# Optimization experiments

Hardware: AMD Instinct MI355X
Metric: run time of the kernel (lower is better)

The kernel has to match this reference:

```python
import jax, jax.numpy as jnp
import numpy as np

B, NPTS, NBASIS, DIM, H, CH = 8, 1024, 8, 8, 512, 16
EPSILON = 1000.0
P = 2
VOLUME = 2.0 ** DIM  # MC domain [-1,1]^dim


def setup_inputs() -> dict:
    key = jax.random.key(0)
    ks = jax.random.split(key, 10)
    s = jax.random.uniform(ks[0], (NPTS, DIM), dtype=jnp.float32) * 2.0 - 1.0  # MC samples in [-1,1]^dim
    x = jax.random.uniform(ks[1], (1, DIM), dtype=jnp.float32) * 2.0 - 1.0     # eval point
    Wfirst = jax.random.normal(ks[2], (DIM, H), dtype=jnp.float32) / np.sqrt(DIM)
    bfirst = jax.random.normal(ks[3], (H,), dtype=jnp.float32) * 0.01
    Wb = jax.random.normal(ks[4], (NBASIS, H, H), dtype=jnp.float32) / np.sqrt(H)
    bb = jax.random.normal(ks[5], (NBASIS, H), dtype=jnp.float32) * 0.01
    Wlast = jax.random.normal(ks[6], (H, CH), dtype=jnp.float32) / np.sqrt(H)
    blast = jax.random.normal(ks[7], (CH,), dtype=jnp.float32) * 0.01
    Wf = jax.random.normal(ks[8], (DIM, CH), dtype=jnp.float32) / np.sqrt(DIM)
    bf = jax.random.normal(ks[9], (CH,), dtype=jnp.float32) * 0.01
    return dict(s=s, x=x, Wfirst=Wfirst, bfirst=bfirst, Wb=Wb, bb=bb,
                Wlast=Wlast, blast=blast, Wf=Wf, bf=bf)


def _basis_all(pts, Wfirst, bfirst, Wb, bb, Wlast, blast):
    # pts: [M, DIM] -> all n basis nets, batch-repeated: [NBASIS, B, M, CH]
    a0 = jax.nn.elu(jnp.einsum('md,dh->mh', pts, Wfirst) + bfirst)          # [M, H]
    a0 = jnp.broadcast_to(a0[None], (B,) + a0.shape)                         # [B, M, H] (repeat over batch)
    a1 = jax.nn.elu(jnp.einsum('bmh,ihk->ibmk', a0, Wb) + bb[:, None, None, :])  # [n, B, M, H]
    return jnp.einsum('ibmk,kc->ibmc', a1, Wlast) + blast                    # [n, B, M, CH]


def reference(s, x, Wfirst, bfirst, Wb, bb, Wlast, blast, Wf, bf):
    # func(s): linear map realizing the projected function  [NPTS, CH]
    f_s = jnp.einsum('nd,dc->nc', s, Wf) + bf
    basis_s = _basis_all(s, Wfirst, bfirst, Wb, bb, Wlast, blast)            # [n, B, NPTS, CH]
    diff = f_s[None, None] - basis_s                                          # broadcast over n, B
    # Monte Carlo integral of (func - basis_i)^p over [-1,1]^dim, per channel
    integral = VOLUME * jnp.mean(diff ** P, axis=-2)                          # [n, B, CH]
    norm_pc = integral ** (1.0 / P)                                           # Lp norm per channel
    norm_b = jnp.sum(jnp.abs(norm_pc) ** P, axis=-1, keepdims=True) ** (1.0 / P)  # [n, B, 1]
    mu = jnp.where(norm_b <= EPSILON, norm_b, 0.0)                            # [n, B, 1]
    basis_x = _basis_all(x, Wfirst, bfirst, Wb, bb, Wlast, blast)[:, :, 0, :]  # [n, B, CH]
    out = jnp.sum(mu * basis_x, axis=0)                                       # [B, CH]
    normalization = 1e-7 + jnp.sum(mu, axis=0)                                # [B, 1]
    return out / normalization
```

## Files before the change

kernel.cpp:

```cpp
#include <hip/hip_runtime.h>

typedef _Float16 half8 __attribute__((ext_vector_type(8)));
typedef float f32x4 __attribute__((ext_vector_type(4)));
typedef float f32x16 __attribute__((ext_vector_type(16)));
typedef unsigned int u32x4 __attribute__((ext_vector_type(4)));

#define NPTS 1024
#define NB 8
#define HDIM 512
#define CH 16
#define RT 1056

#define OFF_WBF 0u
#define OFF_A0F (4u*1024u*1024u)
#define A0SZ    (64u*RT*16u)
#define OFF_WLF (OFF_A0F + A0SZ)
#define OFF_FS  (OFF_WLF + 16384u)
#define OFF_PP  (OFF_FS + 65536u)
#define PPSZ    (8u*4u*RT*16u*4u)
#define OFF_IS  (OFF_PP + PPSZ)
#define OFF_BX  (OFF_IS + 64u)

__device__ __forceinline__ float elu(float z) { return z > 0.f ? z : expm1f(z); }

__global__ __launch_bounds__(256) void kPrep(const float* __restrict__ s,
    const float* __restrict__ x, const float* __restrict__ Wfirst,
    const float* __restrict__ bfirst, const float* __restrict__ Wb,
    const float* __restrict__ Wlast, const float* __restrict__ Wf,
    const float* __restrict__ bf,
    _Float16* __restrict__ Wbf, _Float16* __restrict__ Wlf,
    _Float16* __restrict__ a0f, float* __restrict__ f_s,
    float* __restrict__ Isum) {
  __shared__ __align__(16) float sm[8192];
  int b = blockIdx.x, t = threadIdx.x;
  if (b < 1024) {
    int i = b >> 7, koct = (b >> 1) & 63, n = (b & 1) * 256 + t;
    const float* src = Wb + ((size_t)i * 512 + koct * 8) * 512 + n;
    float v[8];
#pragma unroll
    for (int j = 0; j < 8; ++j) v[j] = src[j * 512];
    union { _Float16 h[8]; u32x4 u; } hu;
#pragma unroll
    for (int j = 0; j < 8; ++j) hu.h[j] = (_Float16)v[j];
    *(u32x4*)(Wbf + ((size_t)(i * 64 + koct) * 512 + n) * 8) = hu.u;
  } else if (b < 1288) {
    int rr = t >> 6, tl = t & 63;
    int m = (b - 1024) * 4 + rr;
    float* sv = &sm[rr * 8];
    if (tl < 8) sv[tl] = (m < 1024) ? s[m * 8 + tl] : (m == 1024 ? x[tl] : 0.f);
    __syncthreads();
    size_t o = ((size_t)tl * RT + m) * 8;
    if (m <= 1024) {
      float acc[8];
#pragma unroll
      for (int jj = 0; jj < 8; ++jj) acc[jj] = bfirst[8 * tl + jj];
#pragma unroll
      for (int d = 0; d < 8; ++d) {
        float sd = sv[d];
        f32x4 w0 = *(const f32x4*)&Wfirst[d * 512 + 8 * tl];
        f32x4 w1 = *(const f32x4*)&Wfirst[d * 512 + 8 * tl + 4];
#pragma unroll
        for (int e = 0; e < 4; ++e) { acc[e] += sd * w0[e]; acc[4 + e] += sd * w1[e]; }
      }
      union { _Float16 h[8]; u32x4 u; } hu;
#pragma unroll
      for (int jj = 0; jj < 8; ++jj) hu.h[jj] = (_Float16)elu(acc[jj]);
      *(u32x4*)(a0f + o) = hu.u;
      if (m < 1024 && tl < 16) {
        float a = bf[tl];
#pragma unroll
        for (int d = 0; d < 8; ++d) a += sv[d] * Wf[d * 16 + tl];
        f_s[m * 16 + tl] = a;
      }
    } else {
      u32x4 z;
#pragma unroll
      for (int e = 0; e < 4; ++e) z[e] = 0u;
      *(u32x4*)(a0f + o) = z;
    }
  } else {
    if (t < 8) Isum[t] = 0.f;
#pragma unroll
    for (int it = 0; it < 32; ++it) sm[t + 256 * it] = Wlast[t + 256 * it];
    __syncthreads();
#pragma unroll
    for (int p = 0; p < 4; ++p) {
      int oi = p * 256 + t;
      int ko = oi >> 4, ch = oi & 15;
      union { _Float16 h[8]; u32x4 u; } hu;
#pragma unroll
      for (int jj = 0; jj < 8; ++jj) hu.h[jj] = (_Float16)sm[(ko * 8 + jj) * 16 + ch];
      *(u32x4*)(Wlf + oi * 8) = hu.u;
    }
  }
}

__global__ __launch_bounds__(256, 4) void kB(const _Float16* __restrict__ Wbf,
    const _Float16* __restrict__ a0f, const _Float16* __restrict__ Wlf,
    const float* __restrict__ bb, float* __restrict__ Pp) {
  __shared__ u32x4 SC[512];
  __shared__ float S2[32][16];
  int t = threadIdx.x, b = blockIdx.x;
  int i = b & 7, r = b >> 3;
  int nq = r & 3, mt = r >> 2;
  int m0 = mt * 32;
  int w = t >> 6, lane = t & 63, ln = lane & 31, q = lane >> 5, q4 = lane >> 4;
  int nw = nq * 128 + w * 32;

  const u32x4* a4 = (const u32x4*)a0f;
  const u32x4* b4 = (const u32x4*)Wbf;
  int ma = m0 + ln, nb = nw + ln, ib = i * 64;

  f32x16 acc;
#pragma unroll
  for (int rr = 0; rr < 16; ++rr) acc[rr] = 0.f;

  u32x4 pa[4][2], pb[4][2];
#pragma unroll
  for (int st = 0; st < 3; ++st) {
    int k0 = st * 4 + q, k1 = k0 + 2;
    pa[st][0] = a4[k0 * RT + ma];
    pa[st][1] = a4[k1 * RT + ma];
    pb[st][0] = b4[(size_t)(ib + k0) * 512 + nb];
    pb[st][1] = b4[(size_t)(ib + k1) * 512 + nb];
  }
#pragma unroll
  for (int ks = 0; ks < 16; ++ks) {
    int sl = ks & 3;
    acc = __builtin_amdgcn_mfma_f32_32x32x16_f16(
        __builtin_bit_cast(half8, pa[sl][0]), __builtin_bit_cast(half8, pb[sl][0]), acc, 0, 0, 0);
    acc = __builtin_amdgcn_mfma_f32_32x32x16_f16(
        __builtin_bit_cast(half8, pa[sl][1]), __builtin_bit_cast(half8, pb[sl][1]), acc, 0, 0, 0);
    if (ks < 13) {
      int sn = (ks + 3) & 3;
      int k0 = (ks + 3) * 4 + q, k1 = k0 + 2;
      pa[sn][0] = a4[k0 * RT + ma];
      pa[sn][1] = a4[k1 * RT + ma];
      pb[sn][0] = b4[(size_t)(ib + k0) * 512 + nb];
      pb[sn][1] = b4[(size_t)(ib + k1) * 512 + nb];
    }
  }

  ((float*)S2)[t] = 0.f;
  ((float*)S2)[t + 256] = 0.f;
  float bcol = bb[i * 512 + nw + ln];
  _Float16* scr = (_Float16*)&SC[w * 128];
#pragma unroll
  for (int rr = 0; rr < 16; ++rr) {
    int row = (rr & 3) + 8 * (rr >> 2) + 4 * q;
    float a1 = elu(acc[rr] + bcol);
    int oi = (row >> 4) * 64 + (ln >> 3) * 16 + (row & 15);
    scr[oi * 8 + (ln & 7)] = (_Float16)a1;
  }
  __syncthreads();

  const u32x4* s4 = &SC[w * 128];
  const u32x4* w4 = (const u32x4*)Wlf;
  int ch = lane & 15;
  half8 wv = __builtin_bit_cast(half8, w4[(size_t)((nw >> 3) + q4) * 16 + ch]);
#pragma unroll
  for (int mt2 = 0; mt2 < 2; ++mt2) {
    f32x4 D2;
#pragma unroll
    for (int rr = 0; rr < 4; ++rr) D2[rr] = 0.f;
    half8 pv = __builtin_bit_cast(half8, s4[mt2 * 64 + q4 * 16 + ch]);
    D2 = __builtin_amdgcn_mfma_f32_16x16x32_f16(pv, wv, D2, 0, 0, 0);
#pragma unroll
    for (int rr = 0; rr < 4; ++rr)
      atomicAdd(&S2[mt2 * 16 + q4 * 4 + rr][ch], D2[rr]);
  }
  __syncthreads();
  for (int o = t; o < 512; o += 256) {
    int m = o >> 4, c2 = o & 15;
    Pp[((size_t)(i * 4 + nq) * RT + m0 + m) * 16 + c2] = S2[m][c2];
  }
}

__global__ __launch_bounds__(256) void kRed(const float* __restrict__ Pp,
    const float* __restrict__ f_s, const float* __restrict__ blast,
    float* __restrict__ Isum, float* __restrict__ basisx) {
  __shared__ float wsum[4];
  int b = blockIdx.x, t = threadIdx.x;
  int i = b / 33, mt = b - i * 33;
  const float* P0 = Pp + (size_t)(i * 4) * RT * 16;
  const size_t PS = (size_t)RT * 16;
  if (mt == 32) {
    if (t < 16) {
      size_t o = (size_t)1024 * 16 + t;
      basisx[i * 16 + t] = P0[o] + P0[PS + o] + P0[2 * PS + o] + P0[3 * PS + o] + blast[t];
    }
    return;
  }
  float loc = 0.f;
#pragma unroll
  for (int p = 0; p < 2; ++p) {
    int item = t + p * 256;
    int m = mt * 32 + (item >> 4), ch = item & 15;
    size_t o = (size_t)m * 16 + ch;
    float bs = P0[o] + P0[PS + o] + P0[2 * PS + o] + P0[3 * PS + o] + blast[ch];
    float d = f_s[o] - bs;
    loc += d * d;
  }
  loc += __shfl_xor(loc, 1, 64);
  loc += __shfl_xor(loc, 2, 64);
  loc += __shfl_xor(loc, 4, 64);
  loc += __shfl_xor(loc, 8, 64);
  loc += __shfl_xor(loc, 16, 64);
  loc += __shfl_xor(loc, 32, 64);
  int lane = t & 63, w = t >> 6;
  if (lane == 0) wsum[w] = loc;
  __syncthreads();
  if (t == 0) atomicAdd(&Isum[i], wsum[0] + wsum[1] + wsum[2] + wsum[3]);
}

__global__ __launch_bounds__(128) void kFin(const float* __restrict__ Isum,
    const float* __restrict__ basisx, float* __restrict__ out) {
  __shared__ float muL[8];
  int t = threadIdx.x;
  if (t < 8) {
    float nb = 0.5f * sqrtf(Isum[t]);
    muL[t] = (nb <= 1000.0f) ? nb : 0.f;
  }
  __syncthreads();
  int ch = t & 15;
  float num = 0.f, den = 1e-7f;
#pragma unroll
  for (int i = 0; i < NB; ++i) {
    num += muL[i] * basisx[i * 16 + ch];
    den += muL[i];
  }
  out[t] = num / den;
}

extern "C" void kernel_launch(void* const* d_in, const int* in_sizes, int n_in,
                              void* d_out, int out_size, void* d_ws, size_t ws_size,
                              hipStream_t stream) {
  const float* s      = (const float*)d_in[0];
  const float* x      = (const float*)d_in[1];
  const float* Wfirst = (const float*)d_in[2];
  const float* bfirst = (const float*)d_in[3];
  const float* Wb     = (const float*)d_in[4];
  const float* bb     = (const float*)d_in[5];
  const float* Wlast  = (const float*)d_in[6];
  const float* blast  = (const float*)d_in[7];
  const float* Wf     = (const float*)d_in[8];
  const float* bf     = (const float*)d_in[9];

  char* ws = (char*)d_ws;
  _Float16* Wbf = (_Float16*)(ws + OFF_WBF);
  _Float16* a0f = (_Float16*)(ws + OFF_A0F);
  _Float16* Wlf = (_Float16*)(ws + OFF_WLF);
  float* f_s    = (float*)(ws + OFF_FS);
  float* Pp     = (float*)(ws + OFF_PP);
  float* Isum   = (float*)(ws + OFF_IS);
  float* basisx = (float*)(ws + OFF_BX);
  float* out    = (float*)d_out;

  kPrep<<<1289, 256, 0, stream>>>(s, x, Wfirst, bfirst, Wb, Wlast, Wf, bf,
                                  Wbf, Wlf, a0f, f_s, Isum);
  kB<<<1056, 256, 0, stream>>>(Wbf, a0f, Wlf, bb, Pp);
  kRed<<<264, 256, 0, stream>>>(Pp, f_s, blast, Isum, basisx);
  kFin<<<1, 128, 0, stream>>>(Isum, basisx, out);
}
```

Before: 116.2 us.

## Fuse reduction and finalize into GEMM kernel with full-N tiles per block

Each kB block now computes all 512 hidden columns for its 32-row tile (four accumulators per wave), so the second-layer partial sums stay in shared memory instead of being written to a global partial buffer. The squared-difference reduction and the final mu-weighted combination are folded into the same kernel, with a last-block-done atomic counter replacing the kRed and kFin launches. This removes two launches and the global round trip for partials. In exchange the grid shrinks from 1056 to 264 blocks, register pressure rises (launch bounds lowered to 2), and the per-block Wlast epilogue is serialized over four column groups.

```diff
diff --git a/kernel.cpp b/kernel.cpp
--- a/kernel.cpp
+++ b/kernel.cpp
@@ -16,10 +16,9 @@
 #define A0SZ    (64u*RT*16u)
 #define OFF_WLF (OFF_A0F + A0SZ)
 #define OFF_FS  (OFF_WLF + 16384u)
-#define OFF_PP  (OFF_FS + 65536u)
-#define PPSZ    (8u*4u*RT*16u*4u)
-#define OFF_IS  (OFF_PP + PPSZ)
+#define OFF_IS  (OFF_FS + 65536u)
 #define OFF_BX  (OFF_IS + 64u)
+#define OFF_CT  (OFF_BX + 512u)
 
 __device__ __forceinline__ float elu(float z) { return z > 0.f ? z : expm1f(z); }
 
@@ -30,7 +29,7 @@
     const float* __restrict__ bf,
     _Float16* __restrict__ Wbf, _Float16* __restrict__ Wlf,
     _Float16* __restrict__ a0f, float* __restrict__ f_s,
-    float* __restrict__ Isum) {
+    float* __restrict__ Isum, unsigned* __restrict__ cnt) {
   __shared__ __align__(16) float sm[8192];
   int b = blockIdx.x, t = threadIdx.x;
   if (b < 1024) {
@@ -80,6 +79,7 @@
     }
   } else {
     if (t < 8) Isum[t] = 0.f;
+    if (t == 8) *cnt = 0u;
 #pragma unroll
     for (int it = 0; it < 32; ++it) sm[t + 256 * it] = Wlast[t + 256 * it];
     __syncthreads();
@@ -95,141 +95,151 @@
   }
 }
 
-__global__ __launch_bounds__(256, 4) void kB(const _Float16* __restrict__ Wbf,
+__global__ __launch_bounds__(256, 2) void kB(const _Float16* __restrict__ Wbf,
     const _Float16* __restrict__ a0f, const _Float16* __restrict__ Wlf,
-    const float* __restrict__ bb, float* __restrict__ Pp) {
+    const float* __restrict__ bb, const float* __restrict__ blast,
+    const float* __restrict__ f_s, float* __restrict__ Isum,
+    float* __restrict__ basisx, unsigned* __restrict__ cnt,
+    float* __restrict__ out) {
   __shared__ u32x4 SC[512];
   __shared__ float S2[32][16];
+  __shared__ float wsum[4];
+  __shared__ unsigned oc;
+  __shared__ float muL[8];
   int t = threadIdx.x, b = blockIdx.x;
-  int i = b & 7, r = b >> 3;
-  int nq = r & 3, mt = r >> 2;
+  int i = b & 7, mt = b >> 3;
   int m0 = mt * 32;
   int w = t >> 6, lane = t & 63, ln = lane & 31, q = lane >> 5, q4 = lane >> 4;
-  int nw = nq * 128 + w * 32;
 
   const u32x4* a4 = (const u32x4*)a0f;
   const u32x4* b4 = (const u32x4*)Wbf;
-  int ma = m0 + ln, nb = nw + ln, ib = i * 64;
-
-  f32x16 acc;
-#pragma unroll
-  for (int rr = 0; rr < 16; ++rr) acc[rr] = 0.f;
-
-  u32x4 pa[4][2], pb[4][2];
-#pragma unroll
-  for (int st = 0; st < 3; ++st) {
+  int ma = m0 + ln, ib = i * 64;
+  int nwl = w * 32 + ln;
+
+  f32x16 acc[4];
+#pragma unroll
+  for (int j = 0; j < 4; ++j)
+#pragma unroll
+    for (int rr = 0; rr < 16; ++rr) acc[j][rr] = 0.f;
+
+  u32x4 pa[3][2], pb[3][2][4];
+#pragma unroll
+  for (int st = 0; st < 2; ++st) {
     int k0 = st * 4 + q, k1 = k0 + 2;
     pa[st][0] = a4[k0 * RT + ma];
     pa[st][1] = a4[k1 * RT + ma];
-    pb[st][0] = b4[(size_t)(ib + k0) * 512 + nb];
-    pb[st][1] = b4[(size_t)(ib + k1) * 512 + nb];
+#pragma unroll
+    for (int j = 0; j < 4; ++j) {
+      pb[st][0][j] = b4[(size_t)(ib + k0) * 512 + nwl + 128 * j];
+      pb[st][1][j] = b4[(size_t)(ib + k1) * 512 + nwl + 128 * j];
+    }
   }
 #pragma unroll
   for (int ks = 0; ks < 16; ++ks) {
-    int sl = ks & 3;
-    acc = __builtin_amdgcn_mfma_f32_32x32x16_f16(
-        __builtin_bit_cast(half8, pa[sl][0]), __builtin_bit_cast(half8, pb[sl][0]), acc, 0, 0, 0);
-    acc = __builtin_amdgcn_mfma_f32_32x32x16_f16(
-        __builtin_bit_cast(half8, pa[sl][1]), __builtin_bit_cast(half8, pb[sl][1]), acc, 0, 0, 0);
-    if (ks < 13) {
-      int sn = (ks + 3) & 3;
-      int k0 = (ks + 3) * 4 + q, k1 = k0 + 2;
+    int sl = ks % 3;
+    if (ks < 14) {
+      int sn = (ks + 2) % 3;
+      int k0 = (ks + 2) * 4 + q, k1 = k0 + 2;
       pa[sn][0] = a4[k0 * RT + ma];
       pa[sn][1] = a4[k1 * RT + ma];
-      pb[sn][0] = b4[(size_t)(ib + k0) * 512 + nb];
-      pb[sn][1] = b4[(size_t)(ib + k1) * 512 + nb];
+#pragma unroll
+      for (int j = 0; j < 4; ++j) {
+        pb[sn][0][j] = b4[(size_t)(ib + k0) * 512 + nwl + 128 * j];
+        pb[sn][1][j] = b4[(size_t)(ib + k1) * 512 + nwl + 128 * j];
+      }
+    }
+#pragma unroll
+    for (int sfx = 0; sfx < 2; ++sfx) {
+      half8 aH = __builtin_bit_cast(half8, pa[sl][sfx]);
+#pragma unroll
+      for (int j = 0; j < 4; ++j)
+        acc[j] = __builtin_amdgcn_mfma_f32_32x32x16_f16(
+            aH, __builtin_bit_cast(half8, pb[sl][sfx][j]), acc[j], 0, 0, 0);
     }
   }
 
   ((float*)S2)[t] = 0.f;
   ((float*)S2)[t + 256] = 0.f;
-  float bcol = bb[i * 512 + nw + ln];
+  __syncthreads();
+
   _Float16* scr = (_Float16*)&SC[w * 128];
-#pragma unroll
-  for (int rr = 0; rr < 16; ++rr) {
-    int row = (rr & 3) + 8 * (rr >> 2) + 4 * q;
-    float a1 = elu(acc[rr] + bcol);
-    int oi = (row >> 4) * 64 + (ln >> 3) * 16 + (row & 15);
-    scr[oi * 8 + (ln & 7)] = (_Float16)a1;
-  }
-  __syncthreads();
-
   const u32x4* s4 = &SC[w * 128];
   const u32x4* w4 = (const u32x4*)Wlf;
   int ch = lane & 15;
-  half8 wv = __builtin_bit_cast(half8, w4[(size_t)((nw >> 3) + q4) * 16 + ch]);
-#pragma unroll
-  for (int mt2 = 0; mt2 < 2; ++mt2) {
-    f32x4 D2;
-#pragma unroll
-    for (int rr = 0; rr < 4; ++rr) D2[rr] = 0.f;
-    half8 pv = __builtin_bit_cast(half8, s4[mt2 * 64 + q4 * 16 + ch]);
-    D2 = __builtin_amdgcn_mfma_f32_16x16x32_f16(pv, wv, D2, 0, 0, 0);
-#pragma unroll
-    for (int rr = 0; rr < 4; ++rr)
-      atomicAdd(&S2[mt2 * 16 + q4 * 4 + rr][ch], D2[rr]);
+#pragma unroll
+  for (int j = 0; j < 4; ++j) {
+    int nw = w * 32 + 128 * j;
+    float bcol = bb[i * 512 + nw + ln];
+#pragma unroll
+    for (int rr = 0; rr < 16; ++rr) {
+      int row = (rr & 3) + 8 * (rr >> 2) + 4 * q;
+      float a1 = elu(acc[j][rr] + bcol);
+      int oi = (row >> 4) * 64 + (ln >> 3) * 16 + (row & 15);
+      scr[oi * 8 + (ln & 7)] = (_Float16)a1;
+    }
+    half8 wv = __builtin_bit_cast(half8, w4[(size_t)((nw >> 3) + q4) * 16 + ch]);
+#pragma unroll
+    for (int mt2 = 0; mt2 < 2; ++mt2) {
+      f32x4 D2;
+#pragma unroll
+      for (int rr = 0; rr < 4; ++rr) D2[rr] = 0.f;
+      half8 pv = __builtin_bit_cast(half8, s4[mt2 * 64 + q4 * 16 + ch]);
+      D2 = __builtin_amdgcn_mfma_f32_16x16x32_f16(pv, wv, D2, 0, 0, 0);
+#pragma unroll
+      for (int rr = 0; rr < 4; ++rr)
+        atomicAdd(&S2[mt2 * 16 + q4 * 4 + rr][ch], D2[rr]);
+    }
   }
   __syncthreads();
-  for (int o = t; o < 512; o += 256) {
-    int m = o >> 4, c2 = o & 15;
-    Pp[((size_t)(i * 4 + nq) * RT + m0 + m) * 16 + c2] = S2[m][c2];
-  }
-}
-
-__global__ __launch_bounds__(256) void kRed(const float* __restrict__ Pp,
-    const float* __restrict__ f_s, const float* __restrict__ blast,
-    float* __restrict__ Isum, float* __restrict__ basisx) {
-  __shared__ float wsum[4];
-  int b = blockIdx.x, t = threadIdx.x;
-  int i = b / 33, mt = b - i * 33;
-  const float* P0 = Pp + (size_t)(i * 4) * RT * 16;
-  const size_t PS = (size_t)RT * 16;
+
   if (mt == 32) {
-    if (t < 16) {
-      size_t o = (size_t)1024 * 16 + t;
-      basisx[i * 16 + t] = P0[o] + P0[PS + o] + P0[2 * PS + o] + P0[3 * PS + o] + blast[t];
-    }
-    return;
-  }
-  float loc = 0.f;
-#pragma unroll
-  for (int p = 0; p < 2; ++p) {
-    int item = t + p * 256;
-    int m = mt * 32 + (item >> 4), ch = item & 15;
-    size_t o = (size_t)m * 16 + ch;
-    float bs = P0[o] + P0[PS + o] + P0[2 * PS + o] + P0[3 * PS + o] + blast[ch];
-    float d = f_s[o] - bs;
-    loc += d * d;
-  }
-  loc += __shfl_xor(loc, 1, 64);
-  loc += __shfl_xor(loc, 2, 64);
-  loc += __shfl_xor(loc, 4, 64);
-  loc += __shfl_xor(loc, 8, 64);
-  loc += __shfl_xor(loc, 16, 64);
-  loc += __shfl_xor(loc, 32, 64);
-  int lane = t & 63, w = t >> 6;
-  if (lane == 0) wsum[w] = loc;
+    if (t < 16) basisx[i * 16 + t] = S2[0][t] + blast[t];
+  } else {
+    float loc = 0.f;
+#pragma unroll
+    for (int p = 0; p < 2; ++p) {
+      int item = t + p * 256;
+      int ml = item >> 4, c2 = item & 15;
+      float bs = S2[ml][c2] + blast[c2];
+      float d = f_s[(size_t)(m0 + ml) * 16 + c2] - bs;
+      loc += d * d;
+    }
+    loc += __shfl_xor(loc, 1, 64);
+    loc += __shfl_xor(loc, 2, 64);
+    loc += __shfl_xor(loc, 4, 64);
+    loc += __shfl_xor(loc, 8, 64);
+    loc += __shfl_xor(loc, 16, 64);
+    loc += __shfl_xor(loc, 32, 64);
+    if (lane == 0) wsum[w] = loc;
+    __syncthreads();
+    if (t == 0) atomicAdd(&Isum[i], wsum[0] + wsum[1] + wsum[2] + wsum[3]);
+  }
+
+  if (t == 0) {
+    __threadfence();
+    oc = atomicAdd(cnt, 1u);
+  }
   __syncthreads();
-  if (t == 0) atomicAdd(&Isum[i], wsum[0] + wsum[1] + wsum[2] + wsum[3]);
-}
-
-__global__ __launch_bounds__(128) void kFin(const float* __restrict__ Isum,
-    const float* __restrict__ basisx, float* __restrict__ out) {
-  __shared__ float muL[8];
-  int t = threadIdx.x;
-  if (t < 8) {
-    float nb = 0.5f * sqrtf(Isum[t]);
-    muL[t] = (nb <= 1000.0f) ? nb : 0.f;
-  }
-  __syncthreads();
-  int ch = t & 15;
-  float num = 0.f, den = 1e-7f;
-#pragma unroll
-  for (int i = 0; i < NB; ++i) {
-    num += muL[i] * basisx[i * 16 + ch];
-    den += muL[i];
-  }
-  out[t] = num / den;
+  if (oc == 263) {
+    __threadfence();
+    if (t < 8) {
+      float S = atomicAdd(&Isum[t], 0.f);
+      float nb = 0.5f * sqrtf(S);
+      muL[t] = (nb <= 1000.0f) ? nb : 0.f;
+    }
+    __syncthreads();
+    if (t < 128) {
+      int c2 = t & 15;
+      float num = 0.f, den = 1e-7f;
+#pragma unroll
+      for (int ii = 0; ii < NB; ++ii) {
+        float bx = atomicAdd(&basisx[ii * 16 + c2], 0.f);
+        num += muL[ii] * bx;
+        den += muL[ii];
+      }
+      out[t] = num / den;
+    }
+  }
 }
 
 extern "C" void kernel_launch(void* const* d_in, const int* in_sizes, int n_in,
@@ -251,14 +261,12 @@
   _Float16* a0f = (_Float16*)(ws + OFF_A0F);
   _Float16* Wlf = (_Float16*)(ws + OFF_WLF);
   float* f_s    = (float*)(ws + OFF_FS);
-  float* Pp     = (float*)(ws + OFF_PP);
   float* Isum   = (float*)(ws + OFF_IS);
   float* basisx = (float*)(ws + OFF_BX);
+  unsigned* cnt = (unsigned*)(ws + OFF_CT);
   float* out    = (float*)d_out;
 
   kPrep<<<1289, 256, 0, stream>>>(s, x, Wfirst, bfirst, Wb, Wlast, Wf, bf,
-                                  Wbf, Wlf, a0f, f_s, Isum);
-  kB<<<1056, 256, 0, stream>>>(Wbf, a0f, Wlf, bb, Pp);
-  kRed<<<264, 256, 0, stream>>>(Pp, f_s, blast, Isum, basisx);
-  kFin<<<1, 128, 0, stream>>>(Isum, basisx, out);
+                                  Wbf, Wlf, a0f, f_s, Isum, cnt);
+  kB<<<264, 256, 0, stream>>>(Wbf, a0f, Wlf, bb, blast, f_s, Isum, basisx, cnt, out);
 }
```

After: 131.2 us. 1.13x slower.

## Split first GEMM K dimension across blocks and move ELU+projection into reduction kernel

Applied to the files above, without the earlier changes.

The big GEMM kernel now splits the 512-wide K reduction in two, doubling the block count to 2112. Each block writes raw fp32 partial accumulators to a new workspace buffer instead of applying bias, ELU and the Wlast projection itself. The reduction kernel sums the two K halves, applies bias and ELU, converts to fp16 in LDS, and runs the full 512-deep projection MFMA before the squared-error reduction. This is meant to raise parallelism and shorten per-block latency in the GEMM. The cost is much more global traffic, since the full fp32 hidden activations are written and re-read, and more work lands in a 264-block reduction kernel.

```diff
diff --git a/kernel.cpp b/kernel.cpp
--- a/kernel.cpp
+++ b/kernel.cpp
@@ -12,14 +12,12 @@
 #define RT 1056
 
 #define OFF_WBF 0u
-#define OFF_A0F (4u*1024u*1024u)
-#define A0SZ    (64u*RT*16u)
-#define OFF_WLF (OFF_A0F + A0SZ)
-#define OFF_FS  (OFF_WLF + 16384u)
-#define OFF_PP  (OFF_FS + 65536u)
-#define PPSZ    (8u*4u*RT*16u*4u)
-#define OFF_IS  (OFF_PP + PPSZ)
-#define OFF_BX  (OFF_IS + 64u)
+#define OFF_A0F 4194304u
+#define OFF_WLF 5275648u
+#define OFF_FS  5292032u
+#define OFF_IS  5357568u
+#define OFF_BX  5357632u
+#define OFF_PZ  5358144u
 
 __device__ __forceinline__ float elu(float z) { return z > 0.f ? z : expm1f(z); }
 
@@ -96,20 +94,19 @@
 }
 
 __global__ __launch_bounds__(256, 4) void kB(const _Float16* __restrict__ Wbf,
-    const _Float16* __restrict__ a0f, const _Float16* __restrict__ Wlf,
-    const float* __restrict__ bb, float* __restrict__ Pp) {
-  __shared__ u32x4 SC[512];
-  __shared__ float S2[32][16];
+    const _Float16* __restrict__ a0f, float* __restrict__ Pz) {
   int t = threadIdx.x, b = blockIdx.x;
-  int i = b & 7, r = b >> 3;
+  int i = b & 7, kq = (b >> 3) & 1, r = b >> 4;
   int nq = r & 3, mt = r >> 2;
   int m0 = mt * 32;
-  int w = t >> 6, lane = t & 63, ln = lane & 31, q = lane >> 5, q4 = lane >> 4;
+  int w = t >> 6, lane = t & 63, ln = lane & 31, q = lane >> 5;
   int nw = nq * 128 + w * 32;
 
   const u32x4* a4 = (const u32x4*)a0f;
   const u32x4* b4 = (const u32x4*)Wbf;
-  int ma = m0 + ln, nb = nw + ln, ib = i * 64;
+  int ma = m0 + ln, nb = nw + ln;
+  int ib = i * 64 + kq * 32;
+  int ka = kq * 32;
 
   f32x16 acc;
 #pragma unroll
@@ -119,86 +116,105 @@
 #pragma unroll
   for (int st = 0; st < 3; ++st) {
     int k0 = st * 4 + q, k1 = k0 + 2;
-    pa[st][0] = a4[k0 * RT + ma];
-    pa[st][1] = a4[k1 * RT + ma];
+    pa[st][0] = a4[(ka + k0) * RT + ma];
+    pa[st][1] = a4[(ka + k1) * RT + ma];
     pb[st][0] = b4[(size_t)(ib + k0) * 512 + nb];
     pb[st][1] = b4[(size_t)(ib + k1) * 512 + nb];
   }
 #pragma unroll
-  for (int ks = 0; ks < 16; ++ks) {
+  for (int ks = 0; ks < 8; ++ks) {
     int sl = ks & 3;
     acc = __builtin_amdgcn_mfma_f32_32x32x16_f16(
         __builtin_bit_cast(half8, pa[sl][0]), __builtin_bit_cast(half8, pb[sl][0]), acc, 0, 0, 0);
     acc = __builtin_amdgcn_mfma_f32_32x32x16_f16(
         __builtin_bit_cast(half8, pa[sl][1]), __builtin_bit_cast(half8, pb[sl][1]), acc, 0, 0, 0);
-    if (ks < 13) {
+    if (ks < 5) {
       int sn = (ks + 3) & 3;
       int k0 = (ks + 3) * 4 + q, k1 = k0 + 2;
-      pa[sn][0] = a4[k0 * RT + ma];
-      pa[sn][1] = a4[k1 * RT + ma];
+      pa[sn][0] = a4[(ka + k0) * RT + ma];
+      pa[sn][1] = a4[(ka + k1) * RT + ma];
       pb[sn][0] = b4[(size_t)(ib + k0) * 512 + nb];
       pb[sn][1] = b4[(size_t)(ib + k1) * 512 + nb];
     }
   }
 
-  ((float*)S2)[t] = 0.f;
-  ((float*)S2)[t + 256] = 0.f;
-  float bcol = bb[i * 512 + nw + ln];
-  _Float16* scr = (_Float16*)&SC[w * 128];
+  size_t base = ((size_t)((i * 33 + mt) * 2 + kq) * 4 + nq) * 4096 + w * 32 + ln;
 #pragma unroll
   for (int rr = 0; rr < 16; ++rr) {
     int row = (rr & 3) + 8 * (rr >> 2) + 4 * q;
-    float a1 = elu(acc[rr] + bcol);
-    int oi = (row >> 4) * 64 + (ln >> 3) * 16 + (row & 15);
-    scr[oi * 8 + (ln & 7)] = (_Float16)a1;
-  }
-  __syncthreads();
-
-  const u32x4* s4 = &SC[w * 128];
+    Pz[base + (size_t)row * 128] = acc[rr];
+  }
+}
+
+__global__ __launch_bounds__(256, 2) void kRed(const float* __restrict__ Pz,
+    const _Float16* __restrict__ Wlf, const float* __restrict__ bb,
+    const float* __restrict__ blast, const float* __restrict__ f_s,
+    float* __restrict__ Isum, float* __restrict__ basisx) {
+  __shared__ __align__(16) char AL[32768];
+  __shared__ float S2f[512];
+  __shared__ float wsum[4];
+  int t = threadIdx.x, b = blockIdx.x;
+  int i = b & 7, mt = b >> 3;
+  int m0 = mt * 32;
+  int w = t >> 6, lane = t & 63, q4 = lane >> 4, ch = lane & 15;
+
+  S2f[t] = 0.f;
+  S2f[t + 256] = 0.f;
+
+  int m = t & 31, og = t >> 5;
+  size_t pzb0 = ((size_t)(i * 33 + mt) * 2) * 4 * 4096;
+  size_t pzb1 = pzb0 + 4 * 4096;
+  u32x4* ALq = (u32x4*)AL;
+#pragma unroll
+  for (int j = 0; j < 8; ++j) {
+    int oct = og + 8 * j;
+    int h0 = oct * 8, nq = h0 >> 7, n0 = h0 & 127;
+    size_t o0 = (size_t)nq * 4096 + m * 128 + n0;
+    f32x4 za0 = *(const f32x4*)&Pz[pzb0 + o0];
+    f32x4 za1 = *(const f32x4*)&Pz[pzb0 + o0 + 4];
+    f32x4 zb0 = *(const f32x4*)&Pz[pzb1 + o0];
+    f32x4 zb1 = *(const f32x4*)&Pz[pzb1 + o0 + 4];
+    union { _Float16 h[8]; u32x4 u; } hu;
+#pragma unroll
+    for (int e = 0; e < 4; ++e) {
+      hu.h[e]     = (_Float16)elu(za0[e] + zb0[e] + bb[i * 512 + h0 + e]);
+      hu.h[4 + e] = (_Float16)elu(za1[e] + zb1[e] + bb[i * 512 + h0 + 4 + e]);
+    }
+    ALq[oct * 32 + m] = hu.u;
+  }
+  __syncthreads();
+
   const u32x4* w4 = (const u32x4*)Wlf;
-  int ch = lane & 15;
-  half8 wv = __builtin_bit_cast(half8, w4[(size_t)((nw >> 3) + q4) * 16 + ch]);
+  float (*S2)[16] = (float(*)[16])S2f;
 #pragma unroll
   for (int mt2 = 0; mt2 < 2; ++mt2) {
     f32x4 D2;
 #pragma unroll
     for (int rr = 0; rr < 4; ++rr) D2[rr] = 0.f;
-    half8 pv = __builtin_bit_cast(half8, s4[mt2 * 64 + q4 * 16 + ch]);
-    D2 = __builtin_amdgcn_mfma_f32_16x16x32_f16(pv, wv, D2, 0, 0, 0);
+#pragma unroll
+    for (int ks2 = 0; ks2 < 4; ++ks2) {
+      int koct = w * 16 + ks2 * 4 + q4;
+      half8 pv = __builtin_bit_cast(half8, ALq[koct * 32 + mt2 * 16 + ch]);
+      half8 wv = __builtin_bit_cast(half8, w4[koct * 16 + ch]);
+      D2 = __builtin_amdgcn_mfma_f32_16x16x32_f16(pv, wv, D2, 0, 0, 0);
+    }
 #pragma unroll
     for (int rr = 0; rr < 4; ++rr)
       atomicAdd(&S2[mt2 * 16 + q4 * 4 + rr][ch], D2[rr]);
   }
   __syncthreads();
-  for (int o = t; o < 512; o += 256) {
-    int m = o >> 4, c2 = o & 15;
-    Pp[((size_t)(i * 4 + nq) * RT + m0 + m) * 16 + c2] = S2[m][c2];
-  }
-}
-
-__global__ __launch_bounds__(256) void kRed(const float* __restrict__ Pp,
-    const float* __restrict__ f_s, const float* __restrict__ blast,
-    float* __restrict__ Isum, float* __restrict__ basisx) {
-  __shared__ float wsum[4];
-  int b = blockIdx.x, t = threadIdx.x;
-  int i = b / 33, mt = b - i * 33;
-  const float* P0 = Pp + (size_t)(i * 4) * RT * 16;
-  const size_t PS = (size_t)RT * 16;
+
   if (mt == 32) {
-    if (t < 16) {
-      size_t o = (size_t)1024 * 16 + t;
-      basisx[i * 16 + t] = P0[o] + P0[PS + o] + P0[2 * PS + o] + P0[3 * PS + o] + blast[t];
-    }
+    if (t < 16) basisx[i * 16 + t] = S2[0][t] + blast[t];
     return;
   }
   float loc = 0.f;
 #pragma unroll
   for (int p = 0; p < 2; ++p) {
-    int item = t + p * 256;
-    int m = mt * 32 + (item >> 4), ch = item & 15;
-    size_t o = (size_t)m * 16 + ch;
-    float bs = P0[o] + P0[PS + o] + P0[2 * PS + o] + P0[3 * PS + o] + blast[ch];
-    float d = f_s[o] - bs;
+    int o = t + 256 * p;
+    int ml = o >> 4, c2 = o & 15;
+    float bs = S2[ml][c2] + blast[c2];
+    float d = f_s[(size_t)(m0 + ml) * 16 + c2] - bs;
     loc += d * d;
   }
   loc += __shfl_xor(loc, 1, 64);
@@ -207,7 +223,6 @@
   loc += __shfl_xor(loc, 8, 64);
   loc += __shfl_xor(loc, 16, 64);
   loc += __shfl_xor(loc, 32, 64);
-  int lane = t & 63, w = t >> 6;
   if (lane == 0) wsum[w] = loc;
   __syncthreads();
   if (t == 0) atomicAdd(&Isum[i], wsum[0] + wsum[1] + wsum[2] + wsum[3]);
@@ -251,14 +266,14 @@
   _Float16* a0f = (_Float16*)(ws + OFF_A0F);
   _Float16* Wlf = (_Float16*)(ws + OFF_WLF);
   float* f_s    = (float*)(ws + OFF_FS);
-  float* Pp     = (float*)(ws + OFF_PP);
   float* Isum   = (float*)(ws + OFF_IS);
   float* basisx = (float*)(ws + OFF_BX);
+  float* Pz     = (float*)(ws + OFF_PZ);
   float* out    = (float*)d_out;
 
   kPrep<<<1289, 256, 0, stream>>>(s, x, Wfirst, bfirst, Wb, Wlast, Wf, bf,
                                   Wbf, Wlf, a0f, f_s, Isum);
-  kB<<<1056, 256, 0, stream>>>(Wbf, a0f, Wlf, bb, Pp);
-  kRed<<<264, 256, 0, stream>>>(Pp, f_s, blast, Isum, basisx);
+  kB<<<2112, 256, 0, stream>>>(Wbf, a0f, Pz);
+  kRed<<<264, 256, 0, stream>>>(Pz, Wlf, bb, blast, f_s, Isum, basisx);
   kFin<<<1, 128, 0, stream>>>(Isum, basisx, out);
 }
```

After: 132.7 us. 1.14x slower.
